# Kernel optimization log

Measured on AMD Instinct MI355X. Metric: run time of the kernel, lower is better.

Reference implementation:

```python
import jax, jax.numpy as jnp
import numpy as np

N_AGENTS = 8
HID = 256            # hidden_size == comm_dim
COMP = 32            # composition_dim
VOCAB = 256          # vocab_size (table has VOCAB+1 rows, last row = EOS token)
T = HID // COMP      # total_tokens = 8
EPSILON = 1e-6
NF = 1.0 / np.sqrt(HID)  # norm_factor


def setup_inputs() -> dict:
    key = jax.random.key(0)
    ks = jax.random.split(key, 12)
    B = 2048 * N_AGENTS  # n_rollout_threads * num_agents
    s = 0.05
    return {
        "hidden_state": jax.random.normal(ks[0], (B, HID), jnp.float32),
        "eps": jax.random.normal(ks[1], (T, B, COMP), jnp.float32),
        "W_Q": jax.random.normal(ks[2], (HID, HID), jnp.float32) * s,
        "b_Q": jnp.zeros((HID,), jnp.float32),
        "W_K": jax.random.normal(ks[3], (HID, HID), jnp.float32) * s,
        "b_K": jnp.zeros((HID,), jnp.float32),
        "W_mu": jax.random.normal(ks[4], (HID, COMP), jnp.float32) * s,
        "b_mu": jnp.zeros((COMP,), jnp.float32),
        "W_var": jax.random.normal(ks[5], (HID, COMP), jnp.float32) * s,
        "b_var": jnp.zeros((COMP,), jnp.float32),
        "vocab": jax.random.uniform(ks[6], (VOCAB + 1, COMP), jnp.float32, minval=-2.0, maxval=2.0),
        "W_sum": jax.random.normal(ks[7], (HID, HID), jnp.float32) * s,
        "b_sum": jnp.zeros((HID,), jnp.float32),
        "W_head": jax.random.normal(ks[8], (HID, HID), jnp.float32) * s,
        "b_head": jnp.zeros((HID,), jnp.float32),
    }


def _forward(hidden_state, eps, W_Q, b_Q, W_K, b_K, W_mu, b_mu, W_var, b_var,
             vocab, W_sum, b_sum, W_head, b_head):
    B = hidden_state.shape[0]
    # NOTE: original code sets V = to_K(hidden_state) (to_V is unused) -- kept faithfully.
    Q = (hidden_state @ W_Q + b_Q) * NF            # [B, HID]
    V = hidden_state @ W_K + b_K                   # [B, HID]
    EOS = vocab[-1]                                # [COMP]

    message = jnp.zeros((B, T, COMP), hidden_state.dtype)
    mask = jnp.ones((B,), hidden_state.dtype)
    finished = jnp.zeros((B,), bool)

    # Sequential recurrence over a small fixed number of tokens (T = 8).
    for i in range(T):
        m = message.reshape(B, HID)
        K = (m @ W_K + b_K) * NF                   # [B, HID]
        attn = jax.nn.softmax(-(Q * K), axis=-1)   # softmin == softmax of negated logits
        hidden_attn = attn * V                     # [B, HID]
        token_mu = hidden_attn @ W_mu + b_mu       # [B, COMP]
        token_log_var = hidden_attn @ W_var + b_var
        token = eps[i] * jnp.exp(0.5 * token_log_var) + token_mu
        # per-dimension min of squared distance over all vocab entries (faithful to torch.min(.,1)[0])
        token = jnp.min((token[:, None, :] - vocab) ** 2, axis=1)  # [B, COMP]
        token = token * mask[:, None]
        eos_hit = jnp.sum((token - EOS) ** 2, axis=-1) < EPSILON   # [B]
        if i > 0:
            prev_hit = jnp.any(
                jnp.sum((token[:, None, :] - message[:, :i]) ** 2, axis=-1) < EPSILON, axis=1)
            hit = jnp.logical_or(prev_hit, eos_hit)
        else:
            hit = eos_hit
        new_eos = jnp.logical_and(hit, jnp.logical_not(finished))
        token = jnp.where(new_eos[:, None], EOS, token)
        mask = jnp.where(hit, jnp.zeros_like(mask), mask)
        finished = jnp.logical_or(finished, hit)
        message = message.at[:, i].set(token)

    comm = message.reshape(B, HID)                 # comm_dim == HID
    b = B // N_AGENTS
    comm = comm.reshape(b, N_AGENTS, HID) / (N_AGENTS - 1)  # comm_mode 'avg'
    # expand to [b, n, n, C] then sum over dim 1 == broadcast total sum to every agent
    comm_sum = jnp.broadcast_to(comm.sum(axis=1, keepdims=True), (b, N_AGENTS, HID))
    comm_sum = comm_sum.reshape(B, HID)
    out = comm_sum @ W_sum + b_sum                 # comm_sum_head
    out = jax.nn.relu(out @ W_head + b_head)       # active_func(comm_head(.))
    return out


def reference(hidden_state, eps, W_Q, b_Q, W_K, b_K, W_mu, b_mu, W_var, b_var,
              vocab, W_sum, b_sum, W_head, b_head):
    return _forward(hidden_state, eps, W_Q, b_Q, W_K, b_K, W_mu, b_mu, W_var, b_var,
                    vocab, W_sum, b_sum, W_head, b_head)
```

## Files before the change

kernel.cpp:

```cpp
#include <hip/hip_runtime.h>

#define ROWSB 32
#define HIDN 256
#define TT 8
#define EPSI 1e-6f
#define HAS 260
#define SVS 260
#define TBSTR 40
#define NCELL 512
#define WS_LUT_F   (32*SVS)
#define WS_DINFO_F (32*SVS + 8192)
#define WS_WMV_F   (32*SVS + 8192 + 64)

__device__ __forceinline__ void ld4(float* d, const float* p) {
  float4 v = *(const float4*)p;
  d[0] = v.x; d[1] = v.y; d[2] = v.z; d[3] = v.w;
}
__device__ __forceinline__ void ld2(float* d, const float* p) {
  float2 v = *(const float2*)p;
  d[0] = v.x; d[1] = v.y;
}
__device__ __forceinline__ void lds_fence() {
  asm volatile("s_waitcnt lgkmcnt(0)" ::: "memory");
}
__device__ __forceinline__ void fma8(float4 wv, float h0, float h1,
                                     float* mu0, float* lv0, float* mu1, float* lv1) {
  mu0[0] += h0*wv.x; lv0[0] += h0*wv.y; mu0[1] += h0*wv.z; lv0[1] += h0*wv.w;
  mu1[0] += h1*wv.x; lv1[0] += h1*wv.y; mu1[1] += h1*wv.z; lv1[1] += h1*wv.w;
}

__global__ __launch_bounds__(256)
void sort_vocab(const float* __restrict__ vocab,
                const float* __restrict__ Wmu, const float* __restrict__ Wvar,
                float* __restrict__ ws) {
  __shared__ float arr[512];
  const int d = blockIdx.x;
  const int t = threadIdx.x;
  ws[WS_WMV_F + ((size_t)t*32 + d)*2 + 0] = Wmu[(size_t)t*32 + d];
  ws[WS_WMV_F + ((size_t)t*32 + d)*2 + 1] = Wvar[(size_t)t*32 + d];
  arr[t] = (t < 257) ? vocab[t*32 + d] : 3.0e38f;
  arr[t+256] = (t == 0) ? vocab[256*32 + d] : 3.0e38f;
  __syncthreads();
  for (int k = 2; k <= 512; k <<= 1) {
    for (int j = k >> 1; j > 0; j >>= 1) {
      #pragma unroll
      for (int h = 0; h < 2; ++h) {
        int i = t + h*256;
        int ixj = i ^ j;
        if (ixj > i) {
          float a = arr[i], b = arr[ixj];
          bool up = ((i & k) == 0);
          if ((a > b) == up) { arr[i] = b; arr[ixj] = a; }
        }
      }
      __syncthreads();
    }
  }
  #pragma unroll
  for (int h = 0; h < 2; ++h) {
    int i = t + h*256;
    if (i < SVS) ws[d*SVS + i] = (i < 257) ? arr[i] : 3.0e38f;
  }
  float base = arr[0];
  float maxv = arr[256];
  float scale = (float)NCELL / fmaxf(maxv - base, 1e-30f);
  if (t == 0) {
    float2* dinfo = (float2*)(ws + WS_DINFO_F);
    dinfo[d] = make_float2(base, scale);
  }
  #pragma unroll
  for (int h = 0; h < 2; ++h) {
    int cell = t + h*256;
    float target = base + (float)cell * (maxv - base) * (1.0f/(float)NCELL);
    int lo = 0, hi = 257;
    while (lo < hi) { int mid = (lo+hi)>>1; if (arr[mid] < target) lo = mid+1; else hi = mid; }
    ((unsigned short*)(ws + WS_LUT_F))[d*NCELL + cell] = (unsigned short)lo;
  }
}

__global__ __launch_bounds__(256) __attribute__((amdgpu_waves_per_eu(2, 2)))
void mac_fused(const float* __restrict__ hs, const float* __restrict__ eps,
               const float* __restrict__ WQ, const float* __restrict__ bQ,
               const float* __restrict__ WK, const float* __restrict__ bK,
               const float* __restrict__ Wmu, const float* __restrict__ bmu,
               const float* __restrict__ Wvar, const float* __restrict__ bvar,
               const float* __restrict__ vocab,
               const float* __restrict__ Wsum, const float* __restrict__ bsum,
               const float* __restrict__ Whead, const float* __restrict__ bhead,
               const float* __restrict__ ws, float* __restrict__ out, int Btot)
{
  __shared__ __align__(16) float ha[ROWSB*HAS];
  __shared__ __align__(16) float vbuf[ROWSB*HAS];
  __shared__ __align__(16) float tokbuf[ROWSB*TBSTR];
  __shared__ float ivbuf[ROWSB], finbuf[ROWSB];

  const int t   = threadIdx.x;
  const int c4  = t & 63;
  const int w   = t >> 6;
  const int rp  = t >> 4;
  const int dp  = t & 15;
  const int d0u = (c4 << 2) & 31;
  const int tg  = c4 >> 3;
  const int rowbase = blockIdx.x * ROWSB;

  float Qr[8][4], Kr[8][4], MSGr[8][4];
  float eosv[4];
  unsigned fin = 0u;

  {
    const float* hp = hs + (size_t)(rowbase + w*8)*HIDN + c4*4;
    #pragma unroll
    for (int rr = 0; rr < 8; ++rr)
      *(float4*)&ha[(w*8+rr)*HAS + c4*4] = *(const float4*)(hp + (size_t)rr*HIDN);
  }
  if (c4 < 8) finbuf[w*8 + c4] = 0.f;
  ld4(eosv, vocab + 256*32 + d0u);
  float dbr[2], dsr[2];
  {
    float t0[4];
    ld4(t0, ws + WS_DINFO_F + dp*4);
    dbr[0]=t0[0]; dsr[0]=t0[1]; dbr[1]=t0[2]; dsr[1]=t0[3];
  }
  float bm[2], bv[2];
  ld2(bm, bmu + dp*2); ld2(bv, bvar + dp*2);
  lds_fence();

  {
    float Vr[8][4];
    {
      float bq[4], bk[4];
      ld4(bq, bQ + c4*4); ld4(bk, bK + c4*4);
      #pragma unroll
      for (int rr = 0; rr < 8; ++rr) {
        #pragma unroll
        for (int k = 0; k < 4; ++k) { Qr[rr][k] = bq[k]; Vr[rr][k] = bk[k]; }
      }
    }
    #pragma unroll 2
    for (int jq = 0; jq < 64; ++jq) {
      float hsq[8][4];
      #pragma unroll
      for (int rr = 0; rr < 8; ++rr) ld4(hsq[rr], &ha[(w*8+rr)*HAS + jq*4]);
      #pragma unroll
      for (int m = 0; m < 4; ++m) {
        float wq[4], wk[4];
        ld4(wq, WQ + (size_t)(jq*4+m)*HIDN + c4*4);
        ld4(wk, WK + (size_t)(jq*4+m)*HIDN + c4*4);
        #pragma unroll
        for (int rr = 0; rr < 8; ++rr) {
          #pragma unroll
          for (int k = 0; k < 4; ++k) {
            Qr[rr][k] += hsq[rr][m]*wq[k];
            Vr[rr][k] += hsq[rr][m]*wk[k];
          }
        }
      }
    }
    #pragma unroll
    for (int rr = 0; rr < 8; ++rr)
      *(float4*)&vbuf[(w*8+rr)*HAS + c4*4] =
          make_float4(Vr[rr][0], Vr[rr][1], Vr[rr][2], Vr[rr][3]);
  }
  {
    float bk[4]; ld4(bk, bK + c4*4);
    #pragma unroll
    for (int rr = 0; rr < 8; ++rr) {
      #pragma unroll
      for (int k = 0; k < 4; ++k) {
        Qr[rr][k] *= (1.0f/256.0f);
        Kr[rr][k]   = bk[k];
        MSGr[rr][k] = 0.f;
      }
    }
  }
  lds_fence();

  for (int it = 0; it < TT; ++it) {
    if (it > 0) {
      const float* Wr = WK + (size_t)((it-1)*32)*HIDN + c4*4;
      #pragma unroll 2
      for (int cq = 0; cq < 8; ++cq) {
        float tq[8][4];
        #pragma unroll
        for (int rr = 0; rr < 8; ++rr) ld4(tq[rr], &tokbuf[(w*8+rr)*TBSTR + cq*4]);
        #pragma unroll
        for (int m = 0; m < 4; ++m) {
          float wv[4]; ld4(wv, Wr + (size_t)(cq*4+m)*HIDN);
          #pragma unroll
          for (int rr = 0; rr < 8; ++rr) {
            #pragma unroll
            for (int k = 0; k < 4; ++k) Kr[rr][k] += tq[rr][m]*wv[k];
          }
        }
      }
    }

    float ep0[2], ep1[2];
    ld2(ep0, eps + ((size_t)it*Btot + rowbase + 2*rp)*32 + dp*2);
    ld2(ep1, eps + ((size_t)it*Btot + rowbase + 2*rp+1)*32 + dp*2);

    #pragma unroll
    for (int rr = 0; rr < 8; ++rr) {
      float e[4]; float s = 0.f;
      #pragma unroll
      for (int k = 0; k < 4; ++k) { e[k] = __expf(-(Qr[rr][k]*Kr[rr][k])); s += e[k]; }
      #pragma unroll
      for (int off = 32; off >= 1; off >>= 1) s += __shfl_xor(s, off);
      if (c4 == rr) ivbuf[w*8+rr] = 1.0f / s;
      float vv[4];
      ld4(vv, &vbuf[(w*8+rr)*HAS + c4*4]);
      *(float4*)&ha[(w*8+rr)*HAS + c4*4] =
          make_float4(e[0]*vv[0], e[1]*vv[1], e[2]*vv[2], e[3]*vv[3]);
    }
    lds_fence();

    float mu0[2]={0,0}, lv0[2]={0,0}, mu1[2]={0,0}, lv1[2]={0,0};
    {
      const float* wmv  = ws + WS_WMV_F + dp*4;
      const float* har0 = &ha[(2*rp)*HAS];
      const float* har1 = &ha[(2*rp+1)*HAS];
      float4 wb0[8], wb1[8];
      #pragma unroll
      for (int u = 0; u < 8; ++u) wb0[u] = *(const float4*)(wmv + (size_t)u*64);
      #pragma unroll 1
      for (int bb = 0; bb < 16; ++bb) {
        {
          const int b = 2*bb;
          float4 h0a = *(const float4*)(har0 + b*8);
          float4 h1a = *(const float4*)(har1 + b*8);
          float4 h0b = *(const float4*)(har0 + b*8 + 4);
          float4 h1b = *(const float4*)(har1 + b*8 + 4);
          const float* wp = wmv + (size_t)(b+1)*512;
          #pragma unroll
          for (int u = 0; u < 8; ++u) wb1[u] = *(const float4*)(wp + (size_t)u*64);
          fma8(wb0[0], h0a.x, h1a.x, mu0, lv0, mu1, lv1);
          fma8(wb0[1], h0a.y, h1a.y, mu0, lv0, mu1, lv1);
          fma8(wb0[2], h0a.z, h1a.z, mu0, lv0, mu1, lv1);
          fma8(wb0[3], h0a.w, h1a.w, mu0, lv0, mu1, lv1);
          fma8(wb0[4], h0b.x, h1b.x, mu0, lv0, mu1, lv1);
          fma8(wb0[5], h0b.y, h1b.y, mu0, lv0, mu1, lv1);
          fma8(wb0[6], h0b.z, h1b.z, mu0, lv0, mu1, lv1);
          fma8(wb0[7], h0b.w, h1b.w, mu0, lv0, mu1, lv1);
        }
        {
          const int b = 2*bb+1;
          float4 h0a = *(const float4*)(har0 + b*8);
          float4 h1a = *(const float4*)(har1 + b*8);
          float4 h0b = *(const float4*)(har0 + b*8 + 4);
          float4 h1b = *(const float4*)(har1 + b*8 + 4);
          if (bb < 15) {
            const float* wp = wmv + (size_t)(b+1)*512;
            #pragma unroll
            for (int u = 0; u < 8; ++u) wb0[u] = *(const float4*)(wp + (size_t)u*64);
          }
          fma8(wb1[0], h0a.x, h1a.x, mu0, lv0, mu1, lv1);
          fma8(wb1[1], h0a.y, h1a.y, mu0, lv0, mu1, lv1);
          fma8(wb1[2], h0a.z, h1a.z, mu0, lv0, mu1, lv1);
          fma8(wb1[3], h0a.w, h1a.w, mu0, lv0, mu1, lv1);
          fma8(wb1[4], h0b.x, h1b.x, mu0, lv0, mu1, lv1);
          fma8(wb1[5], h0b.y, h1b.y, mu0, lv0, mu1, lv1);
          fma8(wb1[6], h0b.z, h1b.z, mu0, lv0, mu1, lv1);
          fma8(wb1[7], h0b.w, h1b.w, mu0, lv0, mu1, lv1);
        }
      }
    }
    {
      float ivr0 = ivbuf[2*rp],  ivr1 = ivbuf[2*rp+1];
      float msk0 = 1.0f - finbuf[2*rp], msk1 = 1.0f - finbuf[2*rp+1];
      const unsigned short* lutg = (const unsigned short*)(ws + WS_LUT_F);
      float md0[2], md1[2];
      #pragma unroll
      for (int d = 0; d < 2; ++d) {
        const int dim = 2*dp + d;
        const float* sp = ws + dim*SVS;
        {
          float mu = mu0[d]*ivr0 + bm[d];
          float lv = lv0[d]*ivr0 + bv[d];
          float x  = ep0[d]*__expf(0.5f*lv) + mu;
          int c = (int)((x - dbr[d]) * dsr[d]);
          c = min(max(c, 0), NCELL-1);
          int idx = (int)lutg[dim*NCELL + c];
          float v = sp[idx];
          while (v < x) { ++idx; v = sp[idx]; }
          float dn = v - x;
          float dpv = (idx > 0) ? (x - sp[idx-1]) : 3.0e38f;
          md0[d] = fminf(dn, dpv);
        }
        {
          float mu = mu1[d]*ivr1 + bm[d];
          float lv = lv1[d]*ivr1 + bv[d];
          float x  = ep1[d]*__expf(0.5f*lv) + mu;
          int c = (int)((x - dbr[d]) * dsr[d]);
          c = min(max(c, 0), NCELL-1);
          int idx = (int)lutg[dim*NCELL + c];
          float v = sp[idx];
          while (v < x) { ++idx; v = sp[idx]; }
          float dn = v - x;
          float dpv = (idx > 0) ? (x - sp[idx-1]) : 3.0e38f;
          md1[d] = fminf(dn, dpv);
        }
      }
      *(float2*)&tokbuf[(2*rp)*TBSTR + dp*2]   = make_float2(md0[0]*md0[0]*msk0, md0[1]*md0[1]*msk0);
      *(float2*)&tokbuf[(2*rp+1)*TBSTR + dp*2] = make_float2(md1[0]*md1[0]*msk1, md1[1]*md1[1]*msk1);
    }
    lds_fence();

    {
      float tokr[8][4];
      #pragma unroll
      for (int rr = 0; rr < 8; ++rr) ld4(tokr[rr], &tokbuf[(w*8+rr)*TBSTR + d0u]);
      unsigned newfin = fin;
      #pragma unroll
      for (int rr = 0; rr < 8; ++rr) {
        float pd = 0.f, ed = 0.f;
        #pragma unroll
        for (int k = 0; k < 4; ++k) { float dm = tokr[rr][k]-MSGr[rr][k]; pd += dm*dm; }
        if (tg == 0) {
          #pragma unroll
          for (int k = 0; k < 4; ++k) { float de = tokr[rr][k]-eosv[k]; ed += de*de; }
        }
        pd += __shfl_xor(pd, 1); ed += __shfl_xor(ed, 1);
        pd += __shfl_xor(pd, 2); ed += __shfl_xor(ed, 2);
        pd += __shfl_xor(pd, 4); ed += __shfl_xor(ed, 4);
        bool lane_hit = (tg < it && pd < EPSI) || (tg == 0 && ed < EPSI);
        bool hit = (__ballot(lane_hit) != 0ull);
        if (hit) {
          if ((tg == it) && !((fin >> rr) & 1u)) {
            #pragma unroll
            for (int k = 0; k < 4; ++k) tokr[rr][k] = eosv[k];
          }
          newfin |= (1u << rr);
        }
        if (tg == it) {
          #pragma unroll
          for (int k = 0; k < 4; ++k) MSGr[rr][k] = tokr[rr][k];
        }
      }
      if (tg == it) {
        #pragma unroll
        for (int rr = 0; rr < 8; ++rr)
          *(float4*)&tokbuf[(w*8+rr)*TBSTR + d0u] =
              make_float4(MSGr[rr][0], MSGr[rr][1], MSGr[rr][2], MSGr[rr][3]);
      }
      if (c4 < 8) finbuf[w*8+c4] = ((newfin >> c4) & 1u) ? 1.f : 0.f;
      fin = newfin;
    }
    lds_fence();
  }

  __syncthreads();
  float* commb = ha;
  float* o1    = ha + 4*HAS;
  {
    float cs[4] = {0,0,0,0};
    #pragma unroll
    for (int rr = 0; rr < 8; ++rr) {
      #pragma unroll
      for (int k = 0; k < 4; ++k) cs[k] += MSGr[rr][k];
    }
    const float i7 = 1.0f/7.0f;
    *(float4*)&commb[w*HAS + c4*4] = make_float4(cs[0]*i7, cs[1]*i7, cs[2]*i7, cs[3]*i7);
  }
  __syncthreads();
  {
    float bs = bsum[t];
    float a1[4] = {bs, bs, bs, bs};
    #pragma unroll 2
    for (int jq = 0; jq < 64; ++jq) {
      float w4[4];
      #pragma unroll
      for (int m = 0; m < 4; ++m) w4[m] = Wsum[(size_t)(jq*4+m)*HIDN + t];
      #pragma unroll
      for (int g = 0; g < 4; ++g) {
        float c[4]; ld4(c, &commb[g*HAS + jq*4]);
        a1[g] += c[0]*w4[0] + c[1]*w4[1] + c[2]*w4[2] + c[3]*w4[3];
      }
    }
    #pragma unroll
    for (int g = 0; g < 4; ++g) o1[g*HAS + t] = a1[g];
  }
  __syncthreads();
  {
    float bh = bhead[t];
    float a2[4] = {bh, bh, bh, bh};
    #pragma unroll 2
    for (int jq = 0; jq < 64; ++jq) {
      float w4[4];
      #pragma unroll
      for (int m = 0; m < 4; ++m) w4[m] = Whead[(size_t)(jq*4+m)*HIDN + t];
      #pragma unroll
      for (int g = 0; g < 4; ++g) {
        float c[4]; ld4(c, &o1[g*HAS + jq*4]);
        a2[g] += c[0]*w4[0] + c[1]*w4[1] + c[2]*w4[2] + c[3]*w4[3];
      }
    }
    #pragma unroll
    for (int g = 0; g < 4; ++g) {
      float r = fmaxf(a2[g], 0.f);
      #pragma unroll
      for (int rr = 0; rr < 8; ++rr)
        out[(size_t)(rowbase + g*8 + rr)*HIDN + t] = r;
    }
  }
}

extern "C" void kernel_launch(void* const* d_in, const int* in_sizes, int n_in,
                              void* d_out, int out_size, void* d_ws, size_t ws_size,
                              hipStream_t stream) {
    const float* hs    = (const float*)d_in[0];
    const float* eps   = (const float*)d_in[1];
    const float* WQ    = (const float*)d_in[2];
    const float* bQ    = (const float*)d_in[3];
    const float* WK    = (const float*)d_in[4];
    const float* bK    = (const float*)d_in[5];
    const float* Wmu   = (const float*)d_in[6];
    const float* bmu   = (const float*)d_in[7];
    const float* Wvar  = (const float*)d_in[8];
    const float* bvar  = (const float*)d_in[9];
    const float* vocab = (const float*)d_in[10];
    const float* Wsum  = (const float*)d_in[11];
    const float* bsum  = (const float*)d_in[12];
    const float* Whead = (const float*)d_in[13];
    const float* bhead = (const float*)d_in[14];
    float* o = (float*)d_out;
    float* wsf = (float*)d_ws;
    int Btot = in_sizes[0] / HIDN;
    hipLaunchKernelGGL(sort_vocab, dim3(32), dim3(256), 0, stream, vocab, Wmu, Wvar, wsf);
    hipLaunchKernelGGL(mac_fused, dim3(Btot / ROWSB), dim3(256), 0, stream,
                       hs, eps, WQ, bQ, WK, bK, Wmu, bmu, Wvar, bvar,
                       vocab, Wsum, bsum, Whead, bhead, wsf, o, Btot);
}
```

Measured before the change: 391.4 us.

## Keep V in registers and drop LDS side buffers to raise occupancy

```diff
diff --git a/kernel.cpp b/kernel.cpp
--- a/kernel.cpp
+++ b/kernel.cpp
@@ -6,7 +6,7 @@
 #define EPSI 1e-6f
 #define HAS 260
 #define SVS 260
-#define TBSTR 40
+#define TBSTR 36
 #define NCELL 512
 #define WS_LUT_F   (32*SVS)
 #define WS_DINFO_F (32*SVS + 8192)
@@ -78,7 +78,7 @@
   }
 }
 
-__global__ __launch_bounds__(256) __attribute__((amdgpu_waves_per_eu(2, 2)))
+__global__ __launch_bounds__(256, 3)
 void mac_fused(const float* __restrict__ hs, const float* __restrict__ eps,
                const float* __restrict__ WQ, const float* __restrict__ bQ,
                const float* __restrict__ WK, const float* __restrict__ bK,
@@ -90,20 +90,19 @@
                const float* __restrict__ ws, float* __restrict__ out, int Btot)
 {
   __shared__ __align__(16) float ha[ROWSB*HAS];
-  __shared__ __align__(16) float vbuf[ROWSB*HAS];
   __shared__ __align__(16) float tokbuf[ROWSB*TBSTR];
-  __shared__ float ivbuf[ROWSB], finbuf[ROWSB];
 
   const int t   = threadIdx.x;
   const int c4  = t & 63;
   const int w   = t >> 6;
   const int rp  = t >> 4;
+  const int lp  = (t >> 4) & 3;
   const int dp  = t & 15;
   const int d0u = (c4 << 2) & 31;
   const int tg  = c4 >> 3;
   const int rowbase = blockIdx.x * ROWSB;
 
-  float Qr[8][4], Kr[8][4], MSGr[8][4];
+  float Qr[8][4], Kr[8][4], Vr[8][4], MSGr[8][4];
   float eosv[4];
   unsigned fin = 0u;
 
@@ -113,7 +112,6 @@
     for (int rr = 0; rr < 8; ++rr)
       *(float4*)&ha[(w*8+rr)*HAS + c4*4] = *(const float4*)(hp + (size_t)rr*HIDN);
   }
-  if (c4 < 8) finbuf[w*8 + c4] = 0.f;
   ld4(eosv, vocab + 256*32 + d0u);
   float dbr[2], dsr[2];
   {
@@ -126,7 +124,6 @@
   lds_fence();
 
   {
-    float Vr[8][4];
     {
       float bq[4], bk[4];
       ld4(bq, bQ + c4*4); ld4(bk, bK + c4*4);
@@ -156,10 +153,6 @@
         }
       }
     }
-    #pragma unroll
-    for (int rr = 0; rr < 8; ++rr)
-      *(float4*)&vbuf[(w*8+rr)*HAS + c4*4] =
-          make_float4(Vr[rr][0], Vr[rr][1], Vr[rr][2], Vr[rr][3]);
   }
   {
     float bk[4]; ld4(bk, bK + c4*4);
@@ -173,23 +166,26 @@
       }
     }
   }
-  lds_fence();
 
   for (int it = 0; it < TT; ++it) {
     if (it > 0) {
       const float* Wr = WK + (size_t)((it-1)*32)*HIDN + c4*4;
       #pragma unroll 2
       for (int cq = 0; cq < 8; ++cq) {
-        float tq[8][4];
         #pragma unroll
-        for (int rr = 0; rr < 8; ++rr) ld4(tq[rr], &tokbuf[(w*8+rr)*TBSTR + cq*4]);
-        #pragma unroll
-        for (int m = 0; m < 4; ++m) {
-          float wv[4]; ld4(wv, Wr + (size_t)(cq*4+m)*HIDN);
-          #pragma unroll
-          for (int rr = 0; rr < 8; ++rr) {
+        for (int h = 0; h < 2; ++h) {
+          float tq[4][4];
+          #pragma unroll
+          for (int r4 = 0; r4 < 4; ++r4)
+            ld4(tq[r4], &tokbuf[(w*8+h*4+r4)*TBSTR + cq*4]);
+          #pragma unroll
+          for (int m = 0; m < 4; ++m) {
+            float wv[4]; ld4(wv, Wr + (size_t)(cq*4+m)*HIDN);
             #pragma unroll
-            for (int k = 0; k < 4; ++k) Kr[rr][k] += tq[rr][m]*wv[k];
+            for (int r4 = 0; r4 < 4; ++r4) {
+              #pragma unroll
+              for (int k = 0; k < 4; ++k) Kr[h*4+r4][k] += tq[r4][m]*wv[k];
+            }
           }
         }
       }
@@ -199,6 +195,7 @@
     ld2(ep0, eps + ((size_t)it*Btot + rowbase + 2*rp)*32 + dp*2);
     ld2(ep1, eps + ((size_t)it*Btot + rowbase + 2*rp+1)*32 + dp*2);
 
+    float iv0 = 0.f, iv1 = 0.f;
     #pragma unroll
     for (int rr = 0; rr < 8; ++rr) {
       float e[4]; float s = 0.f;
@@ -206,11 +203,10 @@
       for (int k = 0; k < 4; ++k) { e[k] = __expf(-(Qr[rr][k]*Kr[rr][k])); s += e[k]; }
       #pragma unroll
       for (int off = 32; off >= 1; off >>= 1) s += __shfl_xor(s, off);
-      if (c4 == rr) ivbuf[w*8+rr] = 1.0f / s;
-      float vv[4];
-      ld4(vv, &vbuf[(w*8+rr)*HAS + c4*4]);
+      if (rr == 2*lp)     iv0 = 1.0f / s;
+      if (rr == 2*lp + 1) iv1 = 1.0f / s;
       *(float4*)&ha[(w*8+rr)*HAS + c4*4] =
-          make_float4(e[0]*vv[0], e[1]*vv[1], e[2]*vv[2], e[3]*vv[3]);
+          make_float4(e[0]*Vr[rr][0], e[1]*Vr[rr][1], e[2]*Vr[rr][2], e[3]*Vr[rr][3]);
     }
     lds_fence();
 
@@ -219,54 +215,42 @@
       const float* wmv  = ws + WS_WMV_F + dp*4;
       const float* har0 = &ha[(2*rp)*HAS];
       const float* har1 = &ha[(2*rp+1)*HAS];
-      float4 wb0[8], wb1[8];
-      #pragma unroll
-      for (int u = 0; u < 8; ++u) wb0[u] = *(const float4*)(wmv + (size_t)u*64);
+      float4 wb0[4], wb1[4];
+      #pragma unroll
+      for (int u = 0; u < 4; ++u) wb0[u] = *(const float4*)(wmv + (size_t)u*64);
       #pragma unroll 1
-      for (int bb = 0; bb < 16; ++bb) {
+      for (int bb = 0; bb < 32; ++bb) {
         {
           const int b = 2*bb;
-          float4 h0a = *(const float4*)(har0 + b*8);
-          float4 h1a = *(const float4*)(har1 + b*8);
-          float4 h0b = *(const float4*)(har0 + b*8 + 4);
-          float4 h1b = *(const float4*)(har1 + b*8 + 4);
-          const float* wp = wmv + (size_t)(b+1)*512;
-          #pragma unroll
-          for (int u = 0; u < 8; ++u) wb1[u] = *(const float4*)(wp + (size_t)u*64);
-          fma8(wb0[0], h0a.x, h1a.x, mu0, lv0, mu1, lv1);
-          fma8(wb0[1], h0a.y, h1a.y, mu0, lv0, mu1, lv1);
-          fma8(wb0[2], h0a.z, h1a.z, mu0, lv0, mu1, lv1);
-          fma8(wb0[3], h0a.w, h1a.w, mu0, lv0, mu1, lv1);
-          fma8(wb0[4], h0b.x, h1b.x, mu0, lv0, mu1, lv1);
-          fma8(wb0[5], h0b.y, h1b.y, mu0, lv0, mu1, lv1);
-          fma8(wb0[6], h0b.z, h1b.z, mu0, lv0, mu1, lv1);
-          fma8(wb0[7], h0b.w, h1b.w, mu0, lv0, mu1, lv1);
+          float4 h0 = *(const float4*)(har0 + b*4);
+          float4 h1 = *(const float4*)(har1 + b*4);
+          const float* wp = wmv + (size_t)(b+1)*256;
+          #pragma unroll
+          for (int u = 0; u < 4; ++u) wb1[u] = *(const float4*)(wp + (size_t)u*64);
+          fma8(wb0[0], h0.x, h1.x, mu0, lv0, mu1, lv1);
+          fma8(wb0[1], h0.y, h1.y, mu0, lv0, mu1, lv1);
+          fma8(wb0[2], h0.z, h1.z, mu0, lv0, mu1, lv1);
+          fma8(wb0[3], h0.w, h1.w, mu0, lv0, mu1, lv1);
         }
         {
           const int b = 2*bb+1;
-          float4 h0a = *(const float4*)(har0 + b*8);
-          float4 h1a = *(const float4*)(har1 + b*8);
-          float4 h0b = *(const float4*)(har0 + b*8 + 4);
-          float4 h1b = *(const float4*)(har1 + b*8 + 4);
-          if (bb < 15) {
-            const float* wp = wmv + (size_t)(b+1)*512;
+          float4 h0 = *(const float4*)(har0 + b*4);
+          float4 h1 = *(const float4*)(har1 + b*4);
+          if (bb < 31) {
+            const float* wp = wmv + (size_t)(b+1)*256;
             #pragma unroll
-            for (int u = 0; u < 8; ++u) wb0[u] = *(const float4*)(wp + (size_t)u*64);
+            for (int u = 0; u < 4; ++u) wb0[u] = *(const float4*)(wp + (size_t)u*64);
           }
-          fma8(wb1[0], h0a.x, h1a.x, mu0, lv0, mu1, lv1);
-          fma8(wb1[1], h0a.y, h1a.y, mu0, lv0, mu1, lv1);
-          fma8(wb1[2], h0a.z, h1a.z, mu0, lv0, mu1, lv1);
-          fma8(wb1[3], h0a.w, h1a.w, mu0, lv0, mu1, lv1);
-          fma8(wb1[4], h0b.x, h1b.x, mu0, lv0, mu1, lv1);
-          fma8(wb1[5], h0b.y, h1b.y, mu0, lv0, mu1, lv1);
-          fma8(wb1[6], h0b.z, h1b.z, mu0, lv0, mu1, lv1);
-          fma8(wb1[7], h0b.w, h1b.w, mu0, lv0, mu1, lv1);
+          fma8(wb1[0], h0.x, h1.x, mu0, lv0, mu1, lv1);
+          fma8(wb1[1], h0.y, h1.y, mu0, lv0, mu1, lv1);
+          fma8(wb1[2], h0.z, h1.z, mu0, lv0, mu1, lv1);
+          fma8(wb1[3], h0.w, h1.w, mu0, lv0, mu1, lv1);
         }
       }
     }
     {
-      float ivr0 = ivbuf[2*rp],  ivr1 = ivbuf[2*rp+1];
-      float msk0 = 1.0f - finbuf[2*rp], msk1 = 1.0f - finbuf[2*rp+1];
+      float msk0 = ((fin >> (2*lp))   & 1u) ? 0.f : 1.f;
+      float msk1 = ((fin >> (2*lp+1)) & 1u) ? 0.f : 1.f;
       const unsigned short* lutg = (const unsigned short*)(ws + WS_LUT_F);
       float md0[2], md1[2];
       #pragma unroll
@@ -274,8 +258,8 @@
         const int dim = 2*dp + d;
         const float* sp = ws + dim*SVS;
         {
-          float mu = mu0[d]*ivr0 + bm[d];
-          float lv = lv0[d]*ivr0 + bv[d];
+          float mu = mu0[d]*iv0 + bm[d];
+          float lv = lv0[d]*iv0 + bv[d];
           float x  = ep0[d]*__expf(0.5f*lv) + mu;
           int c = (int)((x - dbr[d]) * dsr[d]);
           c = min(max(c, 0), NCELL-1);
@@ -287,8 +271,8 @@
           md0[d] = fminf(dn, dpv);
         }
         {
-          float mu = mu1[d]*ivr1 + bm[d];
-          float lv = lv1[d]*ivr1 + bv[d];
+          float mu = mu1[d]*iv1 + bm[d];
+          float lv = lv1[d]*iv1 + bv[d];
           float x  = ep1[d]*__expf(0.5f*lv) + mu;
           int c = (int)((x - dbr[d]) * dsr[d]);
           c = min(max(c, 0), NCELL-1);
@@ -342,7 +326,6 @@
           *(float4*)&tokbuf[(w*8+rr)*TBSTR + d0u] =
               make_float4(MSGr[rr][0], MSGr[rr][1], MSGr[rr][2], MSGr[rr][3]);
       }
-      if (c4 < 8) finbuf[w*8+c4] = ((newfin >> c4) & 1u) ? 1.f : 0.f;
       fin = newfin;
     }
     lds_fence();
```

Result: slower. 547.6 us (+39.9%).
